# Optimization experiments

Hardware: AMD Instinct MI355X
Metric: run time of the kernel (lower is better)

Reference implementation:

```python
import jax, jax.numpy as jnp
import numpy as np

N, C, S, K, H, ES, L = 50000, 128, 2048, 64, 128, 256, 5
E = S * ES


def setup_inputs() -> dict:
    key = jax.random.key(0)
    ks = jax.random.split(key, 16)
    lin = lambda k_, i, o: jax.random.normal(k_, (i, o), jnp.float32) * 0.02
    inp = {}
    inp["x"] = jax.random.normal(ks[0], (N, C), jnp.float32)
    inp["log_probs"] = jax.random.normal(ks[1], (S,), jnp.float32)
    inp["node_proj_w"] = lin(ks[2], C, H); inp["node_proj_b"] = jnp.zeros(H, jnp.float32)
    inp["logp_proj_w"] = lin(ks[3], 1, H); inp["logp_proj_b"] = jnp.zeros(H, jnp.float32)
    inp["root_emb"] = jax.random.normal(ks[4], (2, H), jnp.float32) * 0.02
    inp["init_proj_w"] = lin(ks[5], 3 * H, H); inp["init_proj_b"] = jnp.zeros(H, jnp.float32)
    inp["gin_eps"] = jnp.zeros(L, jnp.float32)
    inp["mlp_w1"] = jax.random.normal(ks[6], (L, H, H), jnp.float32) * 0.02
    inp["mlp_b1"] = jnp.zeros((L, H), jnp.float32)
    inp["mlp_w2"] = jax.random.normal(ks[7], (L, H, H), jnp.float32) * 0.02
    inp["mlp_b2"] = jnp.zeros((L, H), jnp.float32)
    inp["mp2_w"] = jax.random.normal(ks[8], (L, 2 * H, H), jnp.float32) * 0.02
    inp["mp2_b"] = jnp.zeros((L, H), jnp.float32)
    inp["bn_gamma"] = jnp.ones((L, H), jnp.float32)
    inp["bn_beta"] = jnp.zeros((L, H), jnp.float32)
    inp["nodes_t"] = jax.random.randint(ks[9], (S, K), 0, N, jnp.int32)
    inp["root_local"] = jax.random.randint(ks[10], (S,), 0, K, jnp.int32)
    inp["edge_index_t"] = jax.random.randint(ks[11], (2, E), 0, K, jnp.int32)
    inp["edge_ptr"] = jnp.arange(S + 1, dtype=jnp.int32) * ES  # uniform ES edges/subgraph
    return inp


def reference(x, log_probs, node_proj_w, node_proj_b, logp_proj_w, logp_proj_b,
              root_emb, init_proj_w, init_proj_b, gin_eps, mlp_w1, mlp_b1,
              mlp_w2, mlp_b2, mp2_w, mp2_b, bn_gamma, bn_beta,
              nodes_t, root_local, edge_index_t, edge_ptr):
    S_, K_ = nodes_t.shape
    N_total = x.shape[0]
    ids = nodes_t.reshape(-1)                      # [S*k] global IDs, -1 = pad
    valid = ids >= 0
    vf = valid.astype(x.dtype)[:, None]            # [S*k,1]
    idc = jnp.maximum(ids, 0)

    # ---- initial features: node_proj(x_v) || logp_proj(log_p) || root_emb ----
    gx = x[idc] * vf                               # [S*k,C]
    lp = jnp.repeat(log_probs, K_)[:, None]        # [S*k,1]
    root_flat = jnp.arange(S_, dtype=jnp.int32) * K_ + root_local
    root_mask = jnp.zeros(S_ * K_, jnp.int32).at[root_flat].set(1)
    h_node = gx @ node_proj_w + node_proj_b
    h_logp = lp @ logp_proj_w + logp_proj_b
    h_root = root_emb[root_mask]
    h = jnp.concatenate([h_node, h_logp, h_root], axis=-1) @ init_proj_w + init_proj_b

    # ---- intra-subgraph edge index in the flat S*k node space ----
    eidx = jnp.arange(edge_index_t.shape[1], dtype=jnp.int32)
    sub_of_edge = jnp.searchsorted(edge_ptr, eidx, side='right').astype(jnp.int32) - 1
    offs = sub_of_edge * K_
    src = edge_index_t[0] + offs
    dst = edge_index_t[1] + offs

    # valid-node counts per original-graph node (for scatter-mean)
    cnt = jax.ops.segment_sum(vf[:, 0], idc, num_segments=N_total)
    inv_cnt = (1.0 / jnp.maximum(cnt, 1.0))[:, None]

    for l in range(L):
        h_res = h
        # MP-1: GINConv  out = MLP((1+eps)*h + sum_{j->i} h_j)
        agg = jax.ops.segment_sum(h[src], dst, num_segments=S_ * K_)
        z = (1.0 + gin_eps[l]) * h + agg
        z = jax.nn.relu(z @ mlp_w1[l] + mlp_b1[l]) @ mlp_w2[l] + mlp_b2[l]
        # MP-2: cross-subgraph scatter-mean over global node IDs, gather back
        x_agg = jax.ops.segment_sum(z * vf, idc, num_segments=N_total) * inv_cnt
        x_cross = x_agg[idc] * vf
        u = jax.nn.relu(jnp.concatenate([z, x_cross], axis=-1) @ mp2_w[l] + mp2_b[l])
        # BatchNorm (batch statistics, biased var)
        mu = u.mean(axis=0)
        var = u.var(axis=0)
        u = (u - mu) * jax.lax.rsqrt(var + 1e-5) * bn_gamma[l] + bn_beta[l]
        h = u + h_res  # residual; dropout is identity in deterministic reference
    return h
```

## Files before the change

kernel.cpp:

```cpp
#include <hip/hip_runtime.h>
#include <cstdint>

#define NN   50000
#define SS   2048
#define KSUB 64
#define HH   128
#define EE   (SS * 256)
#define SKK  (SS * KSUB)
#define LLAY 5
#define NBLK 196

typedef __attribute__((ext_vector_type(8))) short bhalf8;
typedef __attribute__((ext_vector_type(4))) float f32x4;
typedef __attribute__((ext_vector_type(4))) _Float16 half4;

__device__ __forceinline__ ushort f2b(float f) {
  uint u = __builtin_bit_cast(uint, f);
  uint r = (u + 0x7FFFu + ((u >> 16) & 1u)) >> 16;
  return (ushort)r;
}
__device__ __forceinline__ float b2f(ushort u) {
  uint v = ((uint)u) << 16;
  return __builtin_bit_cast(float, v);
}
__device__ __forceinline__ void fsplit(float f, ushort& hi, ushort& lo) {
  hi = f2b(f);
  lo = f2b(f - b2f(hi));
}
__device__ __forceinline__ int zoff(int row, int col) {
  return row * 256 + (((col * 2) & 255) ^ ((row & 7) << 4));
}

__global__ void fold_M_k(const float* __restrict__ Wn, const float* __restrict__ Wi,
                         ushort* __restrict__ Mth, ushort* __restrict__ Mtl) {
  int c = blockIdx.x, n = threadIdx.x;
  float s = 0.f;
  for (int k = 0; k < HH; ++k) s = fmaf(Wn[c * HH + k], Wi[k * HH + n], s);
  ushort hi, lo; fsplit(s, hi, lo);
  Mth[n * HH + c] = hi; Mtl[n * HH + c] = lo;
}

__global__ void fold_vec_k(const float* __restrict__ Wi, const float* __restrict__ wl,
                           const float* __restrict__ bnb, const float* __restrict__ blb,
                           const float* __restrict__ bi, const float* __restrict__ remb,
                           float* __restrict__ vl, float* __restrict__ c0,
                           float* __restrict__ rev) {
  int n = threadIdx.x;
  float svl = 0.f, sc0 = bi[n], r0 = 0.f, r1 = 0.f;
  for (int k = 0; k < HH; ++k) {
    svl = fmaf(wl[k], Wi[(HH + k) * HH + n], svl);
    sc0 = fmaf(bnb[k], Wi[k * HH + n], sc0);
    sc0 = fmaf(blb[k], Wi[(HH + k) * HH + n], sc0);
    r0  = fmaf(remb[k],      Wi[(2 * HH + k) * HH + n], r0);
    r1  = fmaf(remb[HH + k], Wi[(2 * HH + k) * HH + n], r1);
  }
  vl[n] = svl; c0[n] = sc0; rev[n] = r0; rev[HH + n] = r1;
}

__global__ void wconv_k(const float* __restrict__ w1, const float* __restrict__ w2,
                        const float* __restrict__ mp2w,
                        ushort* __restrict__ w1th, ushort* __restrict__ w1tl,
                        ushort* __restrict__ w2th, ushort* __restrict__ w2tl,
                        ushort* __restrict__ mp2th, ushort* __restrict__ mp2tl) {
  int b = blockIdx.x, n = threadIdx.x;
  ushort hi, lo;
  if (b < 640) {
    int l = b >> 7, k = b & 127;
    fsplit(w1[((size_t)l * HH + k) * HH + n], hi, lo);
    w1th[((size_t)l * HH + n) * HH + k] = hi;
    w1tl[((size_t)l * HH + n) * HH + k] = lo;
  } else if (b < 1280) {
    int bb = b - 640; int l = bb >> 7, k = bb & 127;
    fsplit(w2[((size_t)l * HH + k) * HH + n], hi, lo);
    w2th[((size_t)l * HH + n) * HH + k] = hi;
    w2tl[((size_t)l * HH + n) * HH + k] = lo;
  } else {
    int bb = b - 1280; int l = bb >> 8, k = bb & 255;
    fsplit(mp2w[((size_t)l * 256 + k) * HH + n], hi, lo);
    mp2th[((size_t)l * HH + n) * 256 + k] = hi;
    mp2tl[((size_t)l * HH + n) * 256 + k] = lo;
  }
}

__global__ void count_k(const int* __restrict__ idc, int* __restrict__ cnt) {
  int i = blockIdx.x * 256 + threadIdx.x;
  if (i < SKK) atomicAdd(&cnt[idc[i]], 1);
}

__global__ void scan1_k(const int* __restrict__ cnt, int* __restrict__ excl,
                        int* __restrict__ bsum) {
  __shared__ int sh[256];
  const int tid = threadIdx.x;
  const int i = blockIdx.x * 256 + tid;
  int v = (i < NN) ? cnt[i] : 0;
  sh[tid] = v;
  __syncthreads();
#pragma unroll
  for (int off = 1; off < 256; off <<= 1) {
    int t = (tid >= off) ? sh[tid - off] : 0;
    __syncthreads();
    sh[tid] += t;
    __syncthreads();
  }
  excl[i] = sh[tid] - v;
  if (tid == 255) bsum[blockIdx.x] = sh[tid];
}

__global__ void scan2_k(int* __restrict__ bsum, int* __restrict__ boff) {
  __shared__ int sh[256];
  const int tid = threadIdx.x;
  int v = (tid < NBLK) ? bsum[tid] : 0;
  sh[tid] = v;
  __syncthreads();
#pragma unroll
  for (int off = 1; off < 256; off <<= 1) {
    int t = (tid >= off) ? sh[tid - off] : 0;
    __syncthreads();
    sh[tid] += t;
    __syncthreads();
  }
  boff[tid] = sh[tid] - v;
}

__global__ void scan3_k(const int* __restrict__ excl, const int* __restrict__ boff,
                        int* __restrict__ node_ptr) {
  int i = blockIdx.x * 256 + threadIdx.x;
  if (i < NN) node_ptr[i] = excl[i] + boff[blockIdx.x];
  if (i == 0) node_ptr[NN] = SKK;
}

__global__ void fill_rows_k(const int* __restrict__ idc, const int* __restrict__ node_ptr,
                            int* __restrict__ cur, int* __restrict__ rowlist) {
  int i = blockIdx.x * 256 + threadIdx.x;
  if (i < SKK) {
    int id = idc[i];
    int pos = atomicAdd(&cur[id], 1);
    rowlist[node_ptr[id] + pos] = i;
  }
}

__launch_bounds__(256)
__global__ void scatter_mean_k(const ushort* __restrict__ zh,
                               const int* __restrict__ node_ptr,
                               const int* __restrict__ rowlist,
                               ushort* __restrict__ xah) {
  const int tid = threadIdx.x;
  const int n = blockIdx.x * 16 + (tid >> 4);
  if (n >= NN) return;
  const int c8 = (tid & 15) * 8;
  const int p0 = node_ptr[n], p1 = node_ptr[n + 1];
  float s[8] = {0.f, 0.f, 0.f, 0.f, 0.f, 0.f, 0.f, 0.f};
  for (int p = p0; p < p1; ++p) {
    const size_t off = (size_t)rowlist[p] * HH + c8;
    uint4 vh = *(const uint4*)(zh + off);
    const uint hw[4] = {vh.x, vh.y, vh.z, vh.w};
#pragma unroll
    for (int k = 0; k < 4; ++k) {
      s[2 * k]     += b2f((ushort)hw[k]);
      s[2 * k + 1] += b2f((ushort)(hw[k] >> 16));
    }
  }
  const float inv = 1.0f / (float)max(p1 - p0, 1);
  ushort hi[8];
#pragma unroll
  for (int k = 0; k < 8; ++k) hi[k] = f2b(s[k] * inv);
  *(uint4*)(xah + (size_t)n * HH + c8) = *(uint4*)hi;
}

__launch_bounds__(256)
__global__ void presort_k(const int* __restrict__ e_src, const int* __restrict__ e_dst,
                          const int* __restrict__ edge_ptr, int* __restrict__ row_ptr,
                          int* __restrict__ ssrc) {
  __shared__ int cnt[KSUB];
  __shared__ int base[KSUB];
  __shared__ int cur[KSUB];
  const int s = blockIdx.x, tid = threadIdx.x;
  const int p0 = edge_ptr[s], p1 = edge_ptr[s + 1];
  if (tid < KSUB) cnt[tid] = 0;
  __syncthreads();
  for (int e = p0 + tid; e < p1; e += 256) atomicAdd(&cnt[e_dst[e]], 1);
  __syncthreads();
  if (tid == 0) {
    int a = 0;
    for (int d = 0; d < KSUB; ++d) { base[d] = a; a += cnt[d]; }
  }
  __syncthreads();
  if (tid < KSUB) { row_ptr[s * KSUB + tid] = p0 + base[tid]; cur[tid] = base[tid]; }
  if (s == 0 && tid == 0) row_ptr[SS * KSUB] = edge_ptr[SS];
  __syncthreads();
  for (int e = p0 + tid; e < p1; e += 256) {
    int d = e_dst[e];
    int pos = atomicAdd(&cur[d], 1);
    ssrc[p0 + pos] = e_src[e];
  }
}

template <bool FIRST>
__launch_bounds__(256, 4)
__global__ void gin_mega_k(float* __restrict__ h, const _Float16* __restrict__ uh,
                           const float* __restrict__ stats,
                           const float* __restrict__ gamma, const float* __restrict__ beta,
                           const int* __restrict__ row_ptr, const int* __restrict__ ssrc,
                           const float* __restrict__ gin_eps, const int layer,
                           const ushort* __restrict__ B1h, const ushort* __restrict__ B1l,
                           const ushort* __restrict__ B2h, const ushort* __restrict__ B2l,
                           const float* __restrict__ bias1, const float* __restrict__ bias2,
                           ushort* __restrict__ zh) {
  constexpr int LDH = 132;
  __shared__ __align__(16) char smem[KSUB * LDH * 4];
  __shared__ int ssrc_lds[256];
  float*  hl = (float*)smem;
  ushort* Zh = (ushort*)smem;
  ushort* Zl = (ushort*)(smem + KSUB * HH * 2);
  const int s = blockIdx.x, tid = threadIdx.x;
  const size_t base = (size_t)s * KSUB * HH;

  const int e_start = row_ptr[s * KSUB];
  {
    const int e_end = row_ptr[s * KSUB + KSUB];
    for (int e = e_start + tid; e < e_end; e += 256)
      ssrc_lds[e - e_start] = ssrc[e];
  }

  float csc[4], csh[4];
  const int cb = (tid * 4) & 127;
  if constexpr (!FIRST) {
    const float invM = 1.0f / (float)SKK;
#pragma unroll
    for (int e = 0; e < 4; ++e) {
      const float mu = stats[cb + e] * invM;
      const float var = fmaf(-mu, mu, stats[HH + cb + e] * invM);
      const float sc = rsqrtf(var + 1e-5f) * gamma[cb + e];
      csc[e] = sc; csh[e] = fmaf(-mu, sc, beta[cb + e]);
    }
  }
#pragma unroll
  for (int it = 0; it < 8; ++it) {
    const int idx = it * 1024 + tid * 4;
    const int m = idx >> 7, c = idx & 127;
    float4 hv = *(const float4*)&h[base + idx];
    if constexpr (!FIRST) {
      half4 u4 = *(const half4*)&uh[base + idx];
      hv.x += fmaf((float)u4.x, csc[0], csh[0]);
      hv.y += fmaf((float)u4.y, csc[1], csh[1]);
      hv.z += fmaf((float)u4.z, csc[2], csh[2]);
      hv.w += fmaf((float)u4.w, csc[3], csh[3]);
      *(float4*)&h[base + idx] = hv;
    }
    *(float4*)&hl[m * LDH + c] = hv;
  }
  __syncthreads();

  const float ep1 = 1.0f + gin_eps[layer];
  const int d = tid >> 2, q4 = (tid & 3) * 4;
  const int g = s * KSUB + d;
  const int e0 = row_ptr[g], e1 = row_ptr[g + 1];
  float a[32];
  {
    const float* hp0 = &hl[d * LDH + q4];
#pragma unroll
    for (int j = 0; j < 8; ++j) {
      float4 v = *(const float4*)(hp0 + 16 * j);
      a[4 * j + 0] = ep1 * v.x; a[4 * j + 1] = ep1 * v.y;
      a[4 * j + 2] = ep1 * v.z; a[4 * j + 3] = ep1 * v.w;
    }
    for (int e = e0; e < e1; ++e) {
      const float* hp = &hl[ssrc_lds[e - e_start] * LDH + q4];
#pragma unroll
      for (int j = 0; j < 8; ++j) {
        float4 v = *(const float4*)(hp + 16 * j);
        a[4 * j + 0] += v.x; a[4 * j + 1] += v.y;
        a[4 * j + 2] += v.z; a[4 * j + 3] += v.w;
      }
    }
  }
  __syncthreads();

#pragma unroll
  for (int j = 0; j < 8; ++j) {
    ushort th[4], tl[4];
#pragma unroll
    for (int k = 0; k < 4; ++k) fsplit(a[4 * j + k], th[k], tl[k]);
    const int o = zoff(d, q4 + 16 * j);
    *(uint2*)((char*)Zh + o) = *(uint2*)th;
    *(uint2*)((char*)Zl + o) = *(uint2*)tl;
  }
  __syncthreads();

  const int lane = tid & 63, wv = tid >> 6;
  const int fr = lane & 15, quad = lane >> 4;
  const int nj0 = wv * 32 + fr, nj1 = nj0 + 16;

  f32x4 acc[4][2];
#pragma unroll
  for (int i = 0; i < 4; ++i) { acc[i][0] = (f32x4){0,0,0,0}; acc[i][1] = (f32x4){0,0,0,0}; }

#pragma unroll
  for (int ch = 0; ch < 4; ++ch) {
    bhalf8 afh[4], afl[4], bfh[2], bfl[2];
#pragma unroll
    for (int i = 0; i < 4; ++i) {
      const int o = zoff(i * 16 + fr, ch * 32 + quad * 8);
      afh[i] = *(const bhalf8*)((const char*)Zh + o);
      afl[i] = *(const bhalf8*)((const char*)Zl + o);
    }
#pragma unroll
    for (int j = 0; j < 2; ++j) {
      const size_t off = (size_t)(wv * 32 + j * 16 + fr) * HH + ch * 32 + quad * 8;
      bfh[j] = *(const bhalf8*)(B1h + off);
      bfl[j] = *(const bhalf8*)(B1l + off);
    }
#pragma unroll
    for (int i = 0; i < 4; ++i)
#pragma unroll
      for (int j = 0; j < 2; ++j) {
        acc[i][j] = __builtin_amdgcn_mfma_f32_16x16x32_bf16(afh[i], bfh[j], acc[i][j], 0, 0, 0);
        acc[i][j] = __builtin_amdgcn_mfma_f32_16x16x32_bf16(afl[i], bfh[j], acc[i][j], 0, 0, 0);
        acc[i][j] = __builtin_amdgcn_mfma_f32_16x16x32_bf16(afh[i], bfl[j], acc[i][j], 0, 0, 0);
      }
  }
  __syncthreads();

  {
    const float b10 = bias1[nj0], b11 = bias1[nj1];
#pragma unroll
    for (int i = 0; i < 4; ++i)
#pragma unroll
      for (int r = 0; r < 4; ++r) {
        const int row = i * 16 + quad * 4 + r;
        const float o0 = fmaxf(acc[i][0][r] + b10, 0.f);
        const float o1 = fmaxf(acc[i][1][r] + b11, 0.f);
        ushort h0, l0, h1, l1; fsplit(o0, h0, l0); fsplit(o1, h1, l1);
        *(ushort*)((char*)Zh + zoff(row, nj0)) = h0;
        *(ushort*)((char*)Zl + zoff(row, nj0)) = l0;
        *(ushort*)((char*)Zh + zoff(row, nj1)) = h1;
        *(ushort*)((char*)Zl + zoff(row, nj1)) = l1;
      }
  }
  __syncthreads();

#pragma unroll
  for (int i = 0; i < 4; ++i) { acc[i][0] = (f32x4){0,0,0,0}; acc[i][1] = (f32x4){0,0,0,0}; }
#pragma unroll
  for (int ch = 0; ch < 4; ++ch) {
    bhalf8 afh[4], afl[4], bfh[2], bfl[2];
#pragma unroll
    for (int i = 0; i < 4; ++i) {
      const int o = zoff(i * 16 + fr, ch * 32 + quad * 8);
      afh[i] = *(const bhalf8*)((const char*)Zh + o);
      afl[i] = *(const bhalf8*)((const char*)Zl + o);
    }
#pragma unroll
    for (int j = 0; j < 2; ++j) {
      const size_t off = (size_t)(wv * 32 + j * 16 + fr) * HH + ch * 32 + quad * 8;
      bfh[j] = *(const bhalf8*)(B2h + off);
      bfl[j] = *(const bhalf8*)(B2l + off);
    }
#pragma unroll
    for (int i = 0; i < 4; ++i)
#pragma unroll
      for (int j = 0; j < 2; ++j) {
        acc[i][j] = __builtin_amdgcn_mfma_f32_16x16x32_bf16(afh[i], bfh[j], acc[i][j], 0, 0, 0);
        acc[i][j] = __builtin_amdgcn_mfma_f32_16x16x32_bf16(afl[i], bfh[j], acc[i][j], 0, 0, 0);
        acc[i][j] = __builtin_amdgcn_mfma_f32_16x16x32_bf16(afh[i], bfl[j], acc[i][j], 0, 0, 0);
      }
  }
  __syncthreads();

  {
    const float b20 = bias2[nj0], b21 = bias2[nj1];
#pragma unroll
    for (int i = 0; i < 4; ++i)
#pragma unroll
      for (int r = 0; r < 4; ++r) {
        const int row = i * 16 + quad * 4 + r;
        *(ushort*)((char*)Zh + zoff(row, nj0)) = f2b(acc[i][0][r] + b20);
        *(ushort*)((char*)Zh + zoff(row, nj1)) = f2b(acc[i][1][r] + b21);
      }
  }
  __syncthreads();

#pragma unroll
  for (int k = 0; k < 4; ++k) {
    const int gidx = tid * 8 + k * 2048;
    const int row = gidx >> 7;
    const int col = gidx & 127;
    const int o = zoff(row, col);
    *(uint4*)(zh + base + gidx) = *(const uint4*)((const char*)Zh + o);
  }
}

__launch_bounds__(256, 3)
__global__ void mp2_k(const ushort* __restrict__ Ah,
                      const ushort* __restrict__ A2h,
                      const ushort* __restrict__ Bh, const ushort* __restrict__ Bl,
                      const float* __restrict__ bias, _Float16* __restrict__ Cf,
                      const int* __restrict__ idc, float* __restrict__ stats) {
  constexpr int LDP = 40;
  constexpr int LDU = 136;
  __shared__ __align__(16) char smem[35840];
  ushort* Ash = (ushort*)smem;
  ushort* Bsh = (ushort*)(smem + 10240);
  ushort* Bsl = (ushort*)(smem + 20480);
  const int tid = threadIdx.x;
  const int row0 = blockIdx.x * 128;
  const int lane = tid & 63, wv = tid >> 6;
  const int wm = (wv >> 1) * 64, wn = (wv & 1) * 64;
  const int fr = lane & 15, quad = lane >> 4;
  const int sr = tid >> 1;
  const int sc = (tid & 1) * 16;
  const int grow = idc[row0 + sr];

  f32x4 acc[4][4];
#pragma unroll
  for (int i = 0; i < 4; ++i)
#pragma unroll
    for (int j = 0; j < 4; ++j) acc[i][j] = (f32x4){0.f, 0.f, 0.f, 0.f};

  uint4 eA0, eA1, eB0, eB1, eB2, eB3;
  uint4 oA0, oA1, oB0, oB1, oB2, oB3;
  auto aptr = [&](int ch) -> const ushort* {
    if (ch >= 4) return A2h + ((size_t)grow * HH + (ch - 4) * 32 + sc);
    return Ah + ((size_t)(row0 + sr) * HH + ch * 32 + sc);
  };
  auto LE = [&](int ch) {
    const ushort* ph = aptr(ch);
    eA0 = *(const uint4*)(ph); eA1 = *(const uint4*)(ph + 8);
    const size_t off = (size_t)sr * 256 + ch * 32 + sc;
    eB0 = *(const uint4*)(Bh + off); eB1 = *(const uint4*)(Bh + off + 8);
    eB2 = *(const uint4*)(Bl + off); eB3 = *(const uint4*)(Bl + off + 8);
  };
  auto LO = [&](int ch) {
    const ushort* ph = aptr(ch);
    oA0 = *(const uint4*)(ph); oA1 = *(const uint4*)(ph + 8);
    const size_t off = (size_t)sr * 256 + ch * 32 + sc;
    oB0 = *(const uint4*)(Bh + off); oB1 = *(const uint4*)(Bh + off + 8);
    oB2 = *(const uint4*)(Bl + off); oB3 = *(const uint4*)(Bl + off + 8);
  };
  auto STAGE = [&](uint4 a0, uint4 a1,
                   uint4 b0, uint4 b1, uint4 b2, uint4 b3) {
    *(uint4*)&Ash[sr * LDP + sc]     = a0;
    *(uint4*)&Ash[sr * LDP + sc + 8] = a1;
    *(uint4*)&Bsh[sr * LDP + sc]     = b0;
    *(uint4*)&Bsh[sr * LDP + sc + 8] = b1;
    *(uint4*)&Bsl[sr * LDP + sc]     = b2;
    *(uint4*)&Bsl[sr * LDP + sc + 8] = b3;
  };
  auto MFMA_STEP = [&]() {
    bhalf8 afh[4], bfh[4], bfl[4];
#pragma unroll
    for (int i = 0; i < 4; ++i) {
      const int r = (wm + i * 16 + fr) * LDP + quad * 8;
      afh[i] = *(const bhalf8*)&Ash[r];
    }
#pragma unroll
    for (int j = 0; j < 4; ++j) {
      const int r = (wn + j * 16 + fr) * LDP + quad * 8;
      bfh[j] = *(const bhalf8*)&Bsh[r];
      bfl[j] = *(const bhalf8*)&Bsl[r];
    }
#pragma unroll
    for (int i = 0; i < 4; ++i)
#pragma unroll
      for (int j = 0; j < 4; ++j) {
        acc[i][j] = __builtin_amdgcn_mfma_f32_16x16x32_bf16(afh[i], bfh[j], acc[i][j], 0, 0, 0);
        acc[i][j] = __builtin_amdgcn_mfma_f32_16x16x32_bf16(afh[i], bfl[j], acc[i][j], 0, 0, 0);
      }
  };

  LE(0); LO(1);
#pragma unroll
  for (int chp = 0; chp < 4; ++chp) {
    STAGE(eA0, eA1, eB0, eB1, eB2, eB3);
    __syncthreads();
    if (chp < 3) LE(2 * chp + 2);
    MFMA_STEP();
    __syncthreads();
    STAGE(oA0, oA1, oB0, oB1, oB2, oB3);
    __syncthreads();
    if (chp < 3) LO(2 * chp + 3);
    MFMA_STEP();
    __syncthreads();
  }

  _Float16* uT  = (_Float16*)smem;
  float*    ssum = (float*)(smem + 34816);
  float*    ssq  = ssum + HH;
  const int nj[4] = {wn + fr, wn + 16 + fr, wn + 32 + fr, wn + 48 + fr};
  float bb[4];
#pragma unroll
  for (int j = 0; j < 4; ++j) bb[j] = bias[nj[j]];
  float psum[4] = {0.f, 0.f, 0.f, 0.f}, psq[4] = {0.f, 0.f, 0.f, 0.f};
#pragma unroll
  for (int i = 0; i < 4; ++i)
#pragma unroll
    for (int r = 0; r < 4; ++r) {
      const int row = wm + i * 16 + quad * 4 + r;
#pragma unroll
      for (int j = 0; j < 4; ++j) {
        float o = fmaxf(acc[i][j][r] + bb[j], 0.f);
        uT[row * LDU + nj[j]] = (_Float16)o;
        psum[j] += o; psq[j] += o * o;
      }
    }
  ssum[tid] = 0.f;
  __syncthreads();
#pragma unroll
  for (int j = 0; j < 4; ++j) {
    atomicAdd(&ssum[nj[j]], psum[j]);
    atomicAdd(&ssq[nj[j]], psq[j]);
  }
  __syncthreads();
#pragma unroll
  for (int k = 0; k < 8; ++k) {
    const int idx = tid * 8 + k * 2048;
    const int row = idx >> 7;
    const int col = idx & 127;
    *(uint4*)(Cf + (size_t)(row0 + row) * HH + col) = *(const uint4*)(uT + row * LDU + col);
  }
  if (tid < HH) {
    unsafeAtomicAdd(&stats[tid], ssum[tid]);
    unsafeAtomicAdd(&stats[HH + tid], ssq[tid]);
  }
}

__launch_bounds__(256, 3)
__global__ void mgemm0_k(const float* __restrict__ Afp,
                         const ushort* __restrict__ Bh, const ushort* __restrict__ Bl,
                         float* __restrict__ Cf,
                         const int* __restrict__ idc, const float* __restrict__ log_probs,
                         const int* __restrict__ root_local, const float* __restrict__ vl,
                         const float* __restrict__ c0v, const float* __restrict__ rev) {
  constexpr int LDP = 40;
  __shared__ __align__(16) ushort Ash[128 * LDP];
  __shared__ __align__(16) ushort Asl[128 * LDP];
  __shared__ __align__(16) ushort Bsh[128 * LDP];
  __shared__ __align__(16) ushort Bsl[128 * LDP];
  const int tid = threadIdx.x;
  const int row0 = blockIdx.x * 128;
  const int lane = tid & 63, wv = tid >> 6;
  const int wm = (wv >> 1) * 64, wn = (wv & 1) * 64;
  const int fr = lane & 15, quad = lane >> 4;
  const int sr = tid >> 1;
  const int sc = (tid & 1) * 16;
  const int arow = idc[row0 + sr];

  f32x4 acc[4][4];
#pragma unroll
  for (int i = 0; i < 4; ++i)
#pragma unroll
    for (int j = 0; j < 4; ++j) acc[i][j] = (f32x4){0.f, 0.f, 0.f, 0.f};

  float4 pf0, pf1, pf2, pf3;
  uint4  pb0, pb1, pb2, pb3;
  auto LA = [&](int ch) {
    const float* src = Afp + (size_t)arow * HH + ch * 32 + sc;
    pf0 = *(const float4*)(src);     pf1 = *(const float4*)(src + 4);
    pf2 = *(const float4*)(src + 8); pf3 = *(const float4*)(src + 12);
  };
  auto LB = [&](int ch) {
    const size_t off = (size_t)sr * HH + ch * 32 + sc;
    pb0 = *(const uint4*)(Bh + off); pb1 = *(const uint4*)(Bh + off + 8);
    pb2 = *(const uint4*)(Bl + off); pb3 = *(const uint4*)(Bl + off + 8);
  };

  LA(0); LB(0);
#pragma unroll
  for (int ch = 0; ch < 4; ++ch) {
    {
      float fv[16];
      *(float4*)&fv[0]  = pf0; *(float4*)&fv[4]  = pf1;
      *(float4*)&fv[8]  = pf2; *(float4*)&fv[12] = pf3;
      ushort hi[16], lo[16];
#pragma unroll
      for (int e = 0; e < 16; ++e) fsplit(fv[e], hi[e], lo[e]);
      *(uint4*)&Ash[sr * LDP + sc]     = *(uint4*)&hi[0];
      *(uint4*)&Ash[sr * LDP + sc + 8] = *(uint4*)&hi[8];
      *(uint4*)&Asl[sr * LDP + sc]     = *(uint4*)&lo[0];
      *(uint4*)&Asl[sr * LDP + sc + 8] = *(uint4*)&lo[8];
    }
    *(uint4*)&Bsh[sr * LDP + sc]     = pb0;
    *(uint4*)&Bsh[sr * LDP + sc + 8] = pb1;
    *(uint4*)&Bsl[sr * LDP + sc]     = pb2;
    *(uint4*)&Bsl[sr * LDP + sc + 8] = pb3;
    __syncthreads();
    if (ch < 3) { LA(ch + 1); LB(ch + 1); }
    bhalf8 afh[4], afl[4], bfh[4], bfl[4];
#pragma unroll
    for (int i = 0; i < 4; ++i) {
      const int r = (wm + i * 16 + fr) * LDP + quad * 8;
      afh[i] = *(const bhalf8*)&Ash[r];
      afl[i] = *(const bhalf8*)&Asl[r];
    }
#pragma unroll
    for (int j = 0; j < 4; ++j) {
      const int r = (wn + j * 16 + fr) * LDP + quad * 8;
      bfh[j] = *(const bhalf8*)&Bsh[r];
      bfl[j] = *(const bhalf8*)&Bsl[r];
    }
#pragma unroll
    for (int i = 0; i < 4; ++i)
#pragma unroll
      for (int j = 0; j < 4; ++j) {
        acc[i][j] = __builtin_amdgcn_mfma_f32_16x16x32_bf16(afh[i], bfh[j], acc[i][j], 0, 0, 0);
        acc[i][j] = __builtin_amdgcn_mfma_f32_16x16x32_bf16(afl[i], bfh[j], acc[i][j], 0, 0, 0);
        acc[i][j] = __builtin_amdgcn_mfma_f32_16x16x32_bf16(afh[i], bfl[j], acc[i][j], 0, 0, 0);
      }
    __syncthreads();
  }

  const int nj[4] = {wn + fr, wn + 16 + fr, wn + 32 + fr, wn + 48 + fr};
  float c0a[4], vla[4], re0[4], re1[4];
#pragma unroll
  for (int j = 0; j < 4; ++j) {
    c0a[j] = c0v[nj[j]]; vla[j] = vl[nj[j]];
    re0[j] = rev[nj[j]]; re1[j] = rev[HH + nj[j]];
  }
#pragma unroll
  for (int i = 0; i < 4; ++i)
#pragma unroll
    for (int r = 0; r < 4; ++r) {
      const int m = row0 + wm + i * 16 + quad * 4 + r;
      const int s = m >> 6;
      const float lp = log_probs[s];
      const bool isr = (m & 63) == root_local[s];
      const size_t base = (size_t)m * HH;
#pragma unroll
      for (int j = 0; j < 4; ++j)
        Cf[base + nj[j]] = acc[i][j][r] + c0a[j] + lp * vla[j] + (isr ? re1[j] : re0[j]);
    }
}

__launch_bounds__(256)
__global__ void bn_apply_k(const _Float16* __restrict__ u, float* __restrict__ h,
                           const float* __restrict__ stats,
                           const float* __restrict__ gamma, const float* __restrict__ beta) {
  size_t i4 = (size_t)(blockIdx.x * 256 + threadIdx.x) * 4;
  int c = (int)(i4 & 127);
  const float invM = 1.0f / (float)SKK;
  float sc[4], sh[4];
#pragma unroll
  for (int e = 0; e < 4; ++e) {
    const float mu = stats[c + e] * invM;
    const float var = fmaf(-mu, mu, stats[HH + c + e] * invM);
    const float s = rsqrtf(var + 1e-5f) * gamma[c + e];
    sc[e] = s; sh[e] = fmaf(-mu, s, beta[c + e]);
  }
  half4 uv = *(const half4*)(u + i4);
  float4 hv = *(const float4*)(h + i4);
  float4 o;
  o.x = fmaf((float)uv.x, sc[0], sh[0]) + hv.x;
  o.y = fmaf((float)uv.y, sc[1], sh[1]) + hv.y;
  o.z = fmaf((float)uv.z, sc[2], sh[2]) + hv.z;
  o.w = fmaf((float)uv.w, sc[3], sh[3]) + hv.w;
  *(float4*)(h + i4) = o;
}

extern "C" void kernel_launch(void* const* d_in, const int* in_sizes, int n_in,
                              void* d_out, int out_size, void* d_ws, size_t ws_size,
                              hipStream_t stream) {
  const float* x          = (const float*)d_in[0];
  const float* log_probs  = (const float*)d_in[1];
  const float* node_w     = (const float*)d_in[2];
  const float* node_b     = (const float*)d_in[3];
  const float* logp_w     = (const float*)d_in[4];
  const float* logp_b     = (const float*)d_in[5];
  const float* root_emb   = (const float*)d_in[6];
  const float* init_w     = (const float*)d_in[7];
  const float* init_b     = (const float*)d_in[8];
  const float* gin_eps    = (const float*)d_in[9];
  const float* w1         = (const float*)d_in[10];
  const float* b1         = (const float*)d_in[11];
  const float* w2         = (const float*)d_in[12];
  const float* b2         = (const float*)d_in[13];
  const float* mp2w       = (const float*)d_in[14];
  const float* mp2b       = (const float*)d_in[15];
  const float* gamma      = (const float*)d_in[16];
  const float* beta       = (const float*)d_in[17];
  const int*   nodes      = (const int*)d_in[18];
  const int*   root_local = (const int*)d_in[19];
  const int*   edge_idx   = (const int*)d_in[20];
  const int*   edge_ptr   = (const int*)d_in[21];
  float* h = (float*)d_out;

  char* wp = (char*)d_ws;
  auto take = [&](size_t bytes) { char* p = wp; wp += (bytes + 255) & ~(size_t)255; return p; };
  ushort* zh    = (ushort*)take((size_t)SKK * HH * 2);
  _Float16* uh  = (_Float16*)take((size_t)SKK * HH * 2);
  ushort* xah   = (ushort*)take((size_t)NN * HH * 2);
  ushort* Mth   = (ushort*)take((size_t)HH * HH * 2);
  ushort* Mtl   = (ushort*)take((size_t)HH * HH * 2);
  ushort* w1th  = (ushort*)take((size_t)LLAY * HH * HH * 2);
  ushort* w1tl  = (ushort*)take((size_t)LLAY * HH * HH * 2);
  ushort* w2th  = (ushort*)take((size_t)LLAY * HH * HH * 2);
  ushort* w2tl  = (ushort*)take((size_t)LLAY * HH * HH * 2);
  ushort* mp2th = (ushort*)take((size_t)LLAY * HH * 256 * 2);
  ushort* mp2tl = (ushort*)take((size_t)LLAY * HH * 256 * 2);
  float* vl       = (float*)take(HH * 4);
  float* c0v      = (float*)take(HH * 4);
  float* rev      = (float*)take(2 * HH * 4);
  float* bn_stats = (float*)take(LLAY * 2 * HH * 4);
  int*   cnti     = (int*)take((size_t)NN * 4);
  int*   excl     = (int*)take((size_t)NBLK * 256 * 4);
  int*   bsum     = (int*)take(256 * 4);
  int*   boff     = (int*)take(256 * 4);
  int*   node_ptr = (int*)take((size_t)(NN + 1) * 4);
  int*   cur      = (int*)take((size_t)NN * 4);
  int*   rowlist  = (int*)take((size_t)SKK * 4);
  int*   row_ptr  = (int*)take((size_t)(SKK + 1) * 4);
  int*   ssrc     = (int*)take((size_t)EE * 4);

  hipMemsetAsync(cnti, 0, (size_t)NN * 4, stream);
  hipMemsetAsync(cur, 0, (size_t)NN * 4, stream);
  hipMemsetAsync(bn_stats, 0, LLAY * 2 * HH * 4, stream);
  fold_M_k<<<HH, HH, 0, stream>>>(node_w, init_w, Mth, Mtl);
  fold_vec_k<<<1, HH, 0, stream>>>(init_w, logp_w, node_b, logp_b, init_b, root_emb,
                                   vl, c0v, rev);
  wconv_k<<<2560, HH, 0, stream>>>(w1, w2, mp2w, w1th, w1tl, w2th, w2tl, mp2th, mp2tl);
  count_k<<<SKK / 256, 256, 0, stream>>>(nodes, cnti);
  scan1_k<<<NBLK, 256, 0, stream>>>(cnti, excl, bsum);
  scan2_k<<<1, 256, 0, stream>>>(bsum, boff);
  scan3_k<<<NBLK, 256, 0, stream>>>(excl, boff, node_ptr);
  fill_rows_k<<<SKK / 256, 256, 0, stream>>>(nodes, node_ptr, cur, rowlist);
  presort_k<<<SS, 256, 0, stream>>>(edge_idx, edge_idx + EE, edge_ptr, row_ptr, ssrc);

  mgemm0_k<<<SKK / 128, 256, 0, stream>>>(x, Mth, Mtl, h,
                                          nodes, log_probs, root_local, vl, c0v, rev);

  for (int l = 0; l < LLAY; ++l) {
    if (l == 0) {
      gin_mega_k<true><<<SS, 256, 0, stream>>>(h, nullptr, nullptr, nullptr, nullptr,
                                               row_ptr, ssrc, gin_eps, l,
                                               w1th + (size_t)l * HH * HH,
                                               w1tl + (size_t)l * HH * HH,
                                               w2th + (size_t)l * HH * HH,
                                               w2tl + (size_t)l * HH * HH,
                                               b1 + l * HH, b2 + l * HH, zh);
    } else {
      gin_mega_k<false><<<SS, 256, 0, stream>>>(h, uh, bn_stats + (l - 1) * 2 * HH,
                                                gamma + (l - 1) * HH, beta + (l - 1) * HH,
                                                row_ptr, ssrc, gin_eps, l,
                                                w1th + (size_t)l * HH * HH,
                                                w1tl + (size_t)l * HH * HH,
                                                w2th + (size_t)l * HH * HH,
                                                w2tl + (size_t)l * HH * HH,
                                                b1 + l * HH, b2 + l * HH, zh);
    }
    scatter_mean_k<<<(NN + 15) / 16, 256, 0, stream>>>(zh, node_ptr, rowlist, xah);
    mp2_k<<<SKK / 128, 256, 0, stream>>>(zh, xah,
                                         mp2th + (size_t)l * HH * 256,
                                         mp2tl + (size_t)l * HH * 256,
                                         mp2b + l * HH, uh, nodes,
                                         bn_stats + l * 2 * HH);
  }
  bn_apply_k<<<(SKK * HH / 4) / 256, 256, 0, stream>>>(uh, h, bn_stats + 4 * 2 * HH,
                                                       gamma + 4 * HH, beta + 4 * HH);
}
```

Measured before the change: 800.1 us.

## Fuse cross-subgraph scatter-mean into mp2 kernel via per-row recomputed gathers

Removes the separate scatter_mean kernel and the xah intermediate buffer. Each mp2 thread now recomputes the mean for its row's global node by walking the CSR rowlist of zh. It holds the result in registers and feeds it in as the second half of the A operand. This drops one launch per layer and the write/read of xah. The cost is redundant gathers: every row re-reads all rows that share its global ID, about 2.6 on average. It also adds 32 extra live VGPRs under a 3-wave occupancy bound, which could cause spills or lower occupancy.

After: 1.179 ms. +47.4%, slower.

```diff
diff --git a/kernel.cpp b/kernel.cpp
--- a/kernel.cpp
+++ b/kernel.cpp
@@ -140,34 +140,6 @@
 }
 
 __launch_bounds__(256)
-__global__ void scatter_mean_k(const ushort* __restrict__ zh,
-                               const int* __restrict__ node_ptr,
-                               const int* __restrict__ rowlist,
-                               ushort* __restrict__ xah) {
-  const int tid = threadIdx.x;
-  const int n = blockIdx.x * 16 + (tid >> 4);
-  if (n >= NN) return;
-  const int c8 = (tid & 15) * 8;
-  const int p0 = node_ptr[n], p1 = node_ptr[n + 1];
-  float s[8] = {0.f, 0.f, 0.f, 0.f, 0.f, 0.f, 0.f, 0.f};
-  for (int p = p0; p < p1; ++p) {
-    const size_t off = (size_t)rowlist[p] * HH + c8;
-    uint4 vh = *(const uint4*)(zh + off);
-    const uint hw[4] = {vh.x, vh.y, vh.z, vh.w};
-#pragma unroll
-    for (int k = 0; k < 4; ++k) {
-      s[2 * k]     += b2f((ushort)hw[k]);
-      s[2 * k + 1] += b2f((ushort)(hw[k] >> 16));
-    }
-  }
-  const float inv = 1.0f / (float)max(p1 - p0, 1);
-  ushort hi[8];
-#pragma unroll
-  for (int k = 0; k < 8; ++k) hi[k] = f2b(s[k] * inv);
-  *(uint4*)(xah + (size_t)n * HH + c8) = *(uint4*)hi;
-}
-
-__launch_bounds__(256)
 __global__ void presort_k(const int* __restrict__ e_src, const int* __restrict__ e_dst,
                           const int* __restrict__ edge_ptr, int* __restrict__ row_ptr,
                           int* __restrict__ ssrc) {
@@ -392,7 +364,7 @@
 
 __launch_bounds__(256, 3)
 __global__ void mp2_k(const ushort* __restrict__ Ah,
-                      const ushort* __restrict__ A2h,
+                      const int* __restrict__ node_ptr, const int* __restrict__ rowlist,
                       const ushort* __restrict__ Bh, const ushort* __restrict__ Bl,
                       const float* __restrict__ bias, _Float16* __restrict__ Cf,
                       const int* __restrict__ idc, float* __restrict__ stats) {
@@ -411,6 +383,36 @@
   const int sc = (tid & 1) * 16;
   const int grow = idc[row0 + sr];
 
+  uint4 x0a, x0b, x1a, x1b, x2a, x2b, x3a, x3b;
+  {
+    const int p0 = node_ptr[grow], p1 = node_ptr[grow + 1];
+    const float inv = 1.0f / (float)max(p1 - p0, 1);
+#define GATHQ(BASE, RA, RB)                                                   \
+    {                                                                         \
+      float s_[16];                                                           \
+      _Pragma("unroll") for (int k = 0; k < 16; ++k) s_[k] = 0.f;             \
+      for (int p = p0; p < p1; ++p) {                                         \
+        const ushort* zp = Ah + (size_t)rowlist[p] * HH + (BASE) + sc;        \
+        uint4 v0 = *(const uint4*)zp;                                         \
+        uint4 v1 = *(const uint4*)(zp + 8);                                   \
+        const uint w_[8] = {v0.x, v0.y, v0.z, v0.w, v1.x, v1.y, v1.z, v1.w};  \
+        _Pragma("unroll") for (int k = 0; k < 8; ++k) {                       \
+          s_[2 * k]     += b2f((ushort)w_[k]);                                \
+          s_[2 * k + 1] += b2f((ushort)(w_[k] >> 16));                        \
+        }                                                                     \
+      }                                                                       \
+      ushort o_[16];                                                          \
+      _Pragma("unroll") for (int k = 0; k < 16; ++k) o_[k] = f2b(s_[k] * inv);\
+      RA = *(uint4*)&o_[0];                                                   \
+      RB = *(uint4*)&o_[8];                                                   \
+    }
+    GATHQ(0,  x0a, x0b)
+    GATHQ(32, x1a, x1b)
+    GATHQ(64, x2a, x2b)
+    GATHQ(96, x3a, x3b)
+#undef GATHQ
+  }
+
   f32x4 acc[4][4];
 #pragma unroll
   for (int i = 0; i < 4; ++i)
@@ -419,20 +421,22 @@
 
   uint4 eA0, eA1, eB0, eB1, eB2, eB3;
   uint4 oA0, oA1, oB0, oB1, oB2, oB3;
-  auto aptr = [&](int ch) -> const ushort* {
-    if (ch >= 4) return A2h + ((size_t)grow * HH + (ch - 4) * 32 + sc);
-    return Ah + ((size_t)(row0 + sr) * HH + ch * 32 + sc);
-  };
   auto LE = [&](int ch) {
-    const ushort* ph = aptr(ch);
-    eA0 = *(const uint4*)(ph); eA1 = *(const uint4*)(ph + 8);
+    if (ch < 4) {
+      const ushort* ph = Ah + ((size_t)(row0 + sr) * HH + ch * 32 + sc);
+      eA0 = *(const uint4*)(ph); eA1 = *(const uint4*)(ph + 8);
+    } else if (ch == 4) { eA0 = x0a; eA1 = x0b; }
+    else if (ch == 6)   { eA0 = x2a; eA1 = x2b; }
     const size_t off = (size_t)sr * 256 + ch * 32 + sc;
     eB0 = *(const uint4*)(Bh + off); eB1 = *(const uint4*)(Bh + off + 8);
     eB2 = *(const uint4*)(Bl + off); eB3 = *(const uint4*)(Bl + off + 8);
   };
   auto LO = [&](int ch) {
-    const ushort* ph = aptr(ch);
-    oA0 = *(const uint4*)(ph); oA1 = *(const uint4*)(ph + 8);
+    if (ch < 4) {
+      const ushort* ph = Ah + ((size_t)(row0 + sr) * HH + ch * 32 + sc);
+      oA0 = *(const uint4*)(ph); oA1 = *(const uint4*)(ph + 8);
+    } else if (ch == 5) { oA0 = x1a; oA1 = x1b; }
+    else if (ch == 7)   { oA0 = x3a; oA1 = x3b; }
     const size_t off = (size_t)sr * 256 + ch * 32 + sc;
     oB0 = *(const uint4*)(Bh + off); oB1 = *(const uint4*)(Bh + off + 8);
     oB2 = *(const uint4*)(Bl + off); oB3 = *(const uint4*)(Bl + off + 8);
@@ -687,7 +691,6 @@
   auto take = [&](size_t bytes) { char* p = wp; wp += (bytes + 255) & ~(size_t)255; return p; };
   ushort* zh    = (ushort*)take((size_t)SKK * HH * 2);
   _Float16* uh  = (_Float16*)take((size_t)SKK * HH * 2);
-  ushort* xah   = (ushort*)take((size_t)NN * HH * 2);
   ushort* Mth   = (ushort*)take((size_t)HH * HH * 2);
   ushort* Mtl   = (ushort*)take((size_t)HH * HH * 2);
   ushort* w1th  = (ushort*)take((size_t)LLAY * HH * HH * 2);
@@ -746,8 +749,7 @@
                                                 w2tl + (size_t)l * HH * HH,
                                                 b1 + l * HH, b2 + l * HH, zh);
     }
-    scatter_mean_k<<<(NN + 15) / 16, 256, 0, stream>>>(zh, node_ptr, rowlist, xah);
-    mp2_k<<<SKK / 128, 256, 0, stream>>>(zh, xah,
+    mp2_k<<<SKK / 128, 256, 0, stream>>>(zh, node_ptr, rowlist,
                                          mp2th + (size_t)l * HH * 256,
                                          mp2tl + (size_t)l * HH * 256,
                                          mp2b + l * HH, uh, nodes,
```
